# Optimization experiments

Hardware: AMD Instinct MI355X
Metric: run time of the kernel (lower is better)

## Reference

```python
import jax, jax.numpy as jnp
import numpy as np

N, E = 50000, 800000
IN_FEATS, H, F = 128, 2, 64
NEG_SLOPE = 0.2


def _gat_conv(x, W, attn_l, attn_r, bias, src, dst):
    """DGL-style GATConv. x:[N,IN], W:[H*F,IN], attn_l/attn_r:[H,F], bias:[H*F]. Returns [N,H,F]."""
    z = (x @ W.T).reshape(N, H, F)                      # node projections
    el = jnp.einsum('nhf,hf->nh', z, attn_l)            # [N,H]
    er = jnp.einsum('nhf,hf->nh', z, attn_r)            # [N,H]
    e = jax.nn.leaky_relu(el[src] + er[dst], NEG_SLOPE) # [E,H] edge logits
    # edge softmax over incoming edges of each destination node
    m = jax.ops.segment_max(e, dst, num_segments=N)     # [N,H]
    ex = jnp.exp(e - m[dst])
    s = jax.ops.segment_sum(ex, dst, num_segments=N)    # [N,H]
    alpha = ex / s[dst]                                 # [E,H]
    msg = alpha[:, :, None] * z[src]                    # [E,H,F]
    out = jax.ops.segment_sum(msg, dst, num_segments=N) # [N,H,F]
    return out + bias.reshape(1, H, F)


def setup_inputs() -> dict:
    key = jax.random.key(0)
    ks = jax.random.split(key, 10)
    x = jax.random.normal(ks[0], (N, IN_FEATS), dtype=jnp.float32)
    h = jax.random.normal(ks[1], (N, H, F), dtype=jnp.float32)
    src = jax.random.randint(ks[2], (E,), 0, N, dtype=jnp.int32)
    dst = jax.random.randint(ks[3], (E,), 0, N, dtype=jnp.int32)
    sc = 1.0 / np.sqrt(IN_FEATS)
    W = jax.random.normal(ks[4], (3, H * F, IN_FEATS), dtype=jnp.float32) * sc  # r,u,c fc weights
    attn_l = jax.random.normal(ks[5], (3, H, F), dtype=jnp.float32) * 0.1
    attn_r = jax.random.normal(ks[6], (3, H, F), dtype=jnp.float32) * 0.1
    conv_bias = jax.random.normal(ks[7], (3, H * F), dtype=jnp.float32) * 0.02
    gate_bias = jax.random.uniform(ks[8], (3, H, F), dtype=jnp.float32)  # torch.rand init
    return {"x": x, "h": h, "W": W, "attn_l": attn_l, "attn_r": attn_r,
            "conv_bias": conv_bias, "gate_bias": gate_bias, "src": src, "dst": dst}


def reference(x, h, W, attn_l, attn_r, conv_bias, gate_bias, src, dst):
    # r, u, c gates; each GATConv is applied to x (use_hidden=False branch)
    r = jax.nn.sigmoid(_gat_conv(x, W[0], attn_l[0], attn_r[0], conv_bias[0], src, dst) + gate_bias[0])
    u = jax.nn.sigmoid(_gat_conv(x, W[1], attn_l[1], attn_r[1], conv_bias[1], src, dst) + gate_bias[1])
    # note: original computes h_ = r*h but never uses it in this branch (dead code)
    c = jax.nn.sigmoid(_gat_conv(x, W[2], attn_l[2], attn_r[2], conv_bias[2], src, dst) + gate_bias[2])
    new_h = u * h + (1.0 - u) * c
    return new_h
```

## Files before the change

### kernel.cpp

```cpp
#include <hip/hip_runtime.h>
#include <hip/hip_bf16.h>
#include <math.h>

#define NN 50000
#define EE 800000
#define KIN 128
#define HFD 128
#define ZB 256
#define NB 196
#define KBG 1564
#define CAP 56
#define BSH 7

typedef __bf16 bf16_t;
typedef __bf16 bf16x8 __attribute__((ext_vector_type(8)));
typedef float f32x2 __attribute__((ext_vector_type(2)));
typedef float f32x4 __attribute__((ext_vector_type(4)));
typedef unsigned short u16;
typedef unsigned int u32;
typedef unsigned char u8;

__device__ __forceinline__ float ldf(const void* p, size_t i, int isf32) {
    return isf32 ? ((const float*)p)[i] : (float)((const bf16_t*)p)[i];
}
__device__ __forceinline__ bf16x8 load8bf(const void* base, size_t off, int isf32) {
    if (isf32) {
        const float4* p = (const float4*)((const float*)base + off);
        float4 u = p[0], v = p[1];
        bf16x8 r;
        r[0] = (bf16_t)u.x; r[1] = (bf16_t)u.y; r[2] = (bf16_t)u.z; r[3] = (bf16_t)u.w;
        r[4] = (bf16_t)v.x; r[5] = (bf16_t)v.y; r[6] = (bf16_t)v.z; r[7] = (bf16_t)v.w;
        return r;
    }
    return *(const bf16x8*)((const bf16_t*)base + off);
}

__device__ __forceinline__ uint2 pack8f(const float* v) {
    u32 lo = __builtin_amdgcn_cvt_pk_fp8_f32(v[0], v[1], 0u, false);
    lo = __builtin_amdgcn_cvt_pk_fp8_f32(v[2], v[3], lo, true);
    u32 hi = __builtin_amdgcn_cvt_pk_fp8_f32(v[4], v[5], 0u, false);
    hi = __builtin_amdgcn_cvt_pk_fp8_f32(v[6], v[7], hi, true);
    return make_uint2(lo, hi);
}

__global__ __launch_bounds__(256) void k_front(const unsigned short* __restrict__ xw,
                                               const void* __restrict__ W,
                                               const void* __restrict__ attn_l,
                                               const void* __restrict__ attn_r,
                                               u8* __restrict__ bkt,
                                               int* __restrict__ dflag,
                                               bf16_t* __restrict__ walv)
{
    const int b = blockIdx.x, tid = threadIdx.x;
    int i = b * 256 + tid;
    if (i < NN) *(int*)(bkt + ((size_t)i << BSH)) = 0;
    if (b > 8) return;

    __shared__ int cnt;
    if (tid == 0) cnt = 0;
    __syncthreads();
    int c = 0;
    for (int k = tid; k < 2048; k += 256) {
        int e = (xw[k] >> 7) & 0xFF;
        if (e > 150) c++;
    }
    atomicAdd(&cnt, c);
    __syncthreads();
    const int isf32 = (cnt > 20) ? 1 : 0;

    if (b == 0) {
        if (tid == 0) dflag[0] = isf32;
        return;
    }
    const int c8 = b - 1;
    const int side = c8 >> 2, g = (c8 >> 1) & 1, h = c8 & 1;
    const void* attn = side ? attn_r : attn_l;
    const int k = tid;
    if (k < KIN) {
        float acc = 0.f;
        for (int f = 0; f < 64; f++) {
            float wv = ldf(W, ((size_t)(g + 1) * HFD + h * 64 + f) * KIN + k, isf32);
            float av = ldf(attn, (size_t)((g + 1) * 2 + h) * 64 + f, isf32);
            acc += wv * av;
        }
        walv[(size_t)c8 * KIN + k] = (bf16_t)acc;
    }
}

__global__ __launch_bounds__(256) void k_big(const void* __restrict__ x,
                                             const void* __restrict__ W,
                                             const bf16_t* __restrict__ walv,
                                             u8* __restrict__ z8,
                                             float* __restrict__ eln,
                                             float* __restrict__ ern,
                                             const int* __restrict__ src,
                                             const int* __restrict__ dst,
                                             u8* __restrict__ bkt,
                                             const int* __restrict__ dflag)
{
    __shared__ bf16_t wlds[128 * 128];

    const int bx = blockIdx.x;
    if (bx & 1) {
        int base = (bx >> 1) * 1024 + threadIdx.x * 4;
        if (base < EE) {
            int4 s4 = *(const int4*)(src + base);
            int4 d4 = *(const int4*)(dst + base);
            u8* r0 = bkt + ((size_t)d4.x << BSH);
            u8* r1 = bkt + ((size_t)d4.y << BSH);
            u8* r2 = bkt + ((size_t)d4.z << BSH);
            u8* r3 = bkt + ((size_t)d4.w << BSH);
            int p0 = atomicAdd((int*)r0, 1);
            int p1 = atomicAdd((int*)r1, 1);
            int p2 = atomicAdd((int*)r2, 1);
            int p3 = atomicAdd((int*)r3, 1);
            if (p0 < CAP) *(u16*)(r0 + 4 + 2 * p0) = (u16)s4.x;
            if (p1 < CAP) *(u16*)(r1 + 4 + 2 * p1) = (u16)s4.y;
            if (p2 < CAP) *(u16*)(r2 + 4 + 2 * p2) = (u16)s4.z;
            if (p3 < CAP) *(u16*)(r3 + 4 + 2 * p3) = (u16)s4.w;
        }
        return;
    }

    const int isf32 = dflag[0];
    const int tid = threadIdx.x;
    const int gid = bx >> 1;
    const int g   = gid & 1;
    const int grp = gid >> 1;

    for (int c = tid; c < 2048; c += 256) {
        int col = c >> 4, g8 = c & 15;
        bf16x8 v = load8bf(W, ((size_t)(g + 1) * HFD + col) * KIN + g8 * 8, isf32);
        *(bf16x8*)(wlds + (size_t)col * 128 + (g8 ^ (col & 15)) * 8) = v;
    }

    const int wave = tid >> 6;
    const int lane = tid & 63;
    const int quad = lane >> 4;
    const int lm   = lane & 15;

    bf16x8 wb[4];
    if (g == 0) {
        if (lm < 8) {
#pragma unroll
            for (int kk = 0; kk < 4; kk++)
                wb[kk] = *(const bf16x8*)(walv + (size_t)lm * KIN + kk * 32 + quad * 8);
        } else {
#pragma unroll
            for (int kk = 0; kk < 4; kk++)
#pragma unroll
                for (int jj = 0; jj < 8; jj++) wb[kk][jj] = (bf16_t)0.f;
        }
    }

    __syncthreads();

#pragma unroll 1
    for (int m = 0; m < 2; m++) {
        const int node_base = grp * 128 + m * 64 + wave * 16;
        int nld = node_base + lm;
        if (nld > NN - 1) nld = NN - 1;

        bf16x8 a[4];
#pragma unroll
        for (int kk = 0; kk < 4; kk++)
            a[kk] = load8bf(x, (size_t)nld * KIN + kk * 32 + quad * 8, isf32);

        f32x4 acc[8];
#pragma unroll
        for (int t = 0; t < 8; t++) {
            const int wc = t * 16 + lm;
            f32x4 a4 = {0.f, 0.f, 0.f, 0.f};
#pragma unroll
            for (int kk = 0; kk < 4; kk++) {
                bf16x8 b = *(const bf16x8*)(wlds + (size_t)wc * 128 + ((kk * 4 + quad) ^ lm) * 8);
                a4 = __builtin_amdgcn_mfma_f32_16x16x32_bf16(a[kk], b, a4, 0, 0, 0);
            }
            acc[t] = a4;
        }

        if (g == 0) {
            f32x4 sacc = {0.f, 0.f, 0.f, 0.f};
#pragma unroll
            for (int kk = 0; kk < 4; kk++)
                sacc = __builtin_amdgcn_mfma_f32_16x16x32_bf16(a[kk], wb[kk], sacc, 0, 0, 0);
#pragma unroll
            for (int r = 0; r < 4; r++) {
                int nn = node_base + quad * 4 + r;
                if (nn < NN) {
                    if (lm < 4)      eln[(size_t)nn * 4 + lm] = sacc[r];
                    else if (lm < 8) ern[(size_t)nn * 4 + (lm - 4)] = sacc[r];
                }
            }
        }

#pragma unroll
        for (int r = 0; r < 4; r++) {
            float f[8];
#pragma unroll
            for (int t = 0; t < 8; t++) f[t] = acc[t][r];
            uint2 u = pack8f(f);
            int node = node_base + quad * 4 + r;
            if (node < NN)
                *(uint2*)(z8 + (size_t)node * ZB + g * 128 + lm * 8) = u;
        }
    }
}

__global__ __launch_bounds__(256) void k_agg(const u8* __restrict__ z8,
                                             const u8* __restrict__ bkt,
                                             const float* __restrict__ eln,
                                             const float* __restrict__ ern,
                                             const void* __restrict__ conv_bias,
                                             const void* __restrict__ gate_bias,
                                             const void* __restrict__ hin,
                                             void* __restrict__ out,
                                             const int* __restrict__ dflag)
{
    const int isf32 = dflag[0];
    const int wave = threadIdx.x >> 6;
    const int lane = threadIdx.x & 63;
    const int j = ((lane >> 5) << 1) | (lane & 1);
    const int n = blockIdx.x * 4 + wave;
    if (n >= NN) return;
    const u8* rb = bkt + ((size_t)n << BSH);
    int cnt = *(const int*)rb;
    if (cnt > CAP) cnt = CAP;
    const u16* row = (const u16*)(rb + 4);
    const u32* row32 = (const u32*)row;
    const float erj = ern[(size_t)n * 4 + j];
    const u32 zoff = 4 * lane;

    float a0 = 0.f, a1 = 0.f, a2 = 0.f, a3 = 0.f, s = 0.f;
    int i = 0;
    for (; i + 8 <= cnt; i += 8) {
        u32 rr[4];
#pragma unroll
        for (int q = 0; q < 4; q++) rr[q] = row32[(i >> 1) + q];
        int sn[8];
#pragma unroll
        for (int q = 0; q < 4; q++) { sn[2*q] = rr[q] & 0xFFFF; sn[2*q+1] = rr[q] >> 16; }
        u32 zb[8];
#pragma unroll
        for (int q = 0; q < 8; q++)
            zb[q] = *(const u32*)(z8 + (size_t)sn[q] * ZB + zoff);
        float w[8];
#pragma unroll
        for (int q = 0; q < 8; q++) {
            float v = eln[(size_t)sn[q] * 4 + j] + erj;
            v = v > 0.f ? v : 0.2f * v;
            w[q] = __expf(v);
        }
#pragma unroll
        for (int q = 0; q < 8; q++) {
            f32x2 lo = __builtin_amdgcn_cvt_pk_f32_fp8(zb[q], false);
            f32x2 hi = __builtin_amdgcn_cvt_pk_f32_fp8(zb[q], true);
            a0 += w[q] * lo[0];
            a1 += w[q] * lo[1];
            a2 += w[q] * hi[0];
            a3 += w[q] * hi[1];
            s += w[q];
        }
    }
    if (i + 4 <= cnt) {
        u32 rr[2];
#pragma unroll
        for (int q = 0; q < 2; q++) rr[q] = row32[(i >> 1) + q];
        int sn[4];
#pragma unroll
        for (int q = 0; q < 2; q++) { sn[2*q] = rr[q] & 0xFFFF; sn[2*q+1] = rr[q] >> 16; }
        u32 zb[4];
#pragma unroll
        for (int q = 0; q < 4; q++)
            zb[q] = *(const u32*)(z8 + (size_t)sn[q] * ZB + zoff);
#pragma unroll
        for (int q = 0; q < 4; q++) {
            float v = eln[(size_t)sn[q] * 4 + j] + erj;
            v = v > 0.f ? v : 0.2f * v;
            float w = __expf(v);
            f32x2 lo = __builtin_amdgcn_cvt_pk_f32_fp8(zb[q], false);
            f32x2 hi = __builtin_amdgcn_cvt_pk_f32_fp8(zb[q], true);
            a0 += w * lo[0];
            a1 += w * lo[1];
            a2 += w * hi[0];
            a3 += w * hi[1];
            s += w;
        }
        i += 4;
    }
    for (; i < cnt; i++) {
        int sn = row[i];
        u32 zb = *(const u32*)(z8 + (size_t)sn * ZB + zoff);
        float v = eln[(size_t)sn * 4 + j] + erj;
        v = v > 0.f ? v : 0.2f * v;
        float w = __expf(v);
        f32x2 lo = __builtin_amdgcn_cvt_pk_f32_fp8(zb, false);
        f32x2 hi = __builtin_amdgcn_cvt_pk_f32_fp8(zb, true);
        a0 += w * lo[0];
        a1 += w * lo[1];
        a2 += w * hi[0];
        a3 += w * hi[1];
        s += w;
    }

    float inv = (cnt > 0) ? 1.f / fmaxf(s, 1e-30f) : 0.f;
    float o[4] = {a0 * inv, a1 * inv, a2 * inv, a3 * inv};

    const int gate = lane >> 5;
    int cf[4];
#pragma unroll
    for (int u = 0; u < 4; u++) cf[u] = (4 * (lane & 1) + u) * 16 + ((lane & 31) >> 1);

    float res[4];
    float hh[4];
    if (lane < 32) {
#pragma unroll
        for (int u = 0; u < 4; u++)
            hh[u] = ldf(hin, (size_t)n * HFD + cf[u], isf32);
    }
#pragma unroll
    for (int u = 0; u < 4; u++) {
        float ob = ldf(conv_bias, (size_t)(gate + 1) * HFD + cf[u], isf32)
                 + ldf(gate_bias, (size_t)((gate + 1) * 2 + (lane & 1)) * 64 + (cf[u] & 63), isf32);
        float gv = 1.f / (1.f + __expf(-(o[u] + ob)));
        float other = __shfl(gv, lane ^ 32, 64);
        if (lane < 32)
            res[u] = gv * hh[u] + (1.f - gv) * other;
    }
    if (lane < 32) {
        if (isf32) {
#pragma unroll
            for (int u = 0; u < 4; u++)
                ((float*)out)[(size_t)n * HFD + cf[u]] = res[u];
        } else {
#pragma unroll
            for (int u = 0; u < 4; u++)
                ((bf16_t*)out)[(size_t)n * HFD + cf[u]] = (bf16_t)res[u];
        }
    }
}

extern "C" void kernel_launch(void* const* d_in, const int* in_sizes, int n_in,
                              void* d_out, int out_size, void* d_ws, size_t ws_size,
                              hipStream_t stream)
{
    const void* x         = d_in[0];
    const void* hin       = d_in[1];
    const void* W         = d_in[2];
    const void* attn_l    = d_in[3];
    const void* attn_r    = d_in[4];
    const void* conv_bias = d_in[5];
    const void* gate_bias = d_in[6];
    const int* src        = (const int*)d_in[7];
    const int* dst        = (const int*)d_in[8];

    char* p = (char*)d_ws;
    int* dflag    = (int*)p;    p += 256;
    u8* z8        = (u8*)p;     p += (size_t)NN * ZB;
    float* eln    = (float*)p;  p += (size_t)NN * 4 * 4;
    float* ern    = (float*)p;  p += (size_t)NN * 4 * 4;
    u8* bkt       = (u8*)p;     p += (size_t)NN << BSH;
    bf16_t* walv  = (bf16_t*)p; p += 8 * KIN * 2;

    k_front<<<NB, 256, 0, stream>>>((const unsigned short*)x, W, attn_l, attn_r,
                                    bkt, dflag, walv);
    k_big<<<KBG, 256, 0, stream>>>(x, W, walv, z8, eln, ern, src, dst,
                                   bkt, dflag);
    k_agg<<<(NN + 3) / 4, 256, 0, stream>>>(z8, bkt, eln, ern,
                                            conv_bias, gate_bias, hin, d_out, dflag);
}
```

Measured before the change: 232.6 us.

## Split GEMM blocks to 64 nodes, fold log2e into attention, use exp2 and 32-bit offsets

The projection kernel now gives each GEMM block 64 nodes instead of looping over two 64-node chunks. The grid is interleaved 2:1 GEMM-to-bucketing blocks, which doubles the GEMM block count and spreads the edge-bucketing work between them. The log2(e) factor is folded into the precomputed attention-weight vectors, so the aggregation kernel can use exp2f directly. Gather addressing also switches to 32-bit unsigned arithmetic to shave address computation. In exchange, each GEMM block pays the 32KB weight LDS fill for half as much work.

```diff
diff --git a/kernel.cpp b/kernel.cpp
--- a/kernel.cpp
+++ b/kernel.cpp
@@ -8,7 +8,8 @@
 #define HFD 128
 #define ZB 256
 #define NB 196
-#define KBG 1564
+#define GB2 1564
+#define SB 782
 #define CAP 56
 #define BSH 7
 
@@ -83,7 +84,7 @@
             float av = ldf(attn, (size_t)((g + 1) * 2 + h) * 64 + f, isf32);
             acc += wv * av;
         }
-        walv[(size_t)c8 * KIN + k] = (bf16_t)acc;
+        walv[(size_t)c8 * KIN + k] = (bf16_t)(acc * 1.44269504f);
     }
 }
 
@@ -101,8 +102,8 @@
     __shared__ bf16_t wlds[128 * 128];
 
     const int bx = blockIdx.x;
-    if (bx & 1) {
-        int base = (bx >> 1) * 1024 + threadIdx.x * 4;
+    if (bx % 3 == 2) {
+        int base = (bx / 3) * 1024 + threadIdx.x * 4;
         if (base < EE) {
             int4 s4 = *(const int4*)(src + base);
             int4 d4 = *(const int4*)(dst + base);
@@ -124,9 +125,9 @@
 
     const int isf32 = dflag[0];
     const int tid = threadIdx.x;
-    const int gid = bx >> 1;
-    const int g   = gid & 1;
-    const int grp = gid >> 1;
+    const int gid = (bx / 3) * 2 + (bx % 3);
+    const int ng = gid >> 1;
+    const int g  = gid & 1;
 
     for (int c = tid; c < 2048; c += 256) {
         int col = c >> 4, g8 = c & 15;
@@ -138,72 +139,62 @@
     const int lane = tid & 63;
     const int quad = lane >> 4;
     const int lm   = lane & 15;
-
-    bf16x8 wb[4];
+    const int node_base = ng * 64 + wave * 16;
+
+    int nld = node_base + lm;
+    if (nld > NN - 1) nld = NN - 1;
+
+    bf16x8 a[4];
+#pragma unroll
+    for (int kk = 0; kk < 4; kk++)
+        a[kk] = load8bf(x, (size_t)nld * KIN + kk * 32 + quad * 8, isf32);
+
+    __syncthreads();
+
+    f32x4 acc[8];
+#pragma unroll
+    for (int t = 0; t < 8; t++) {
+        const int wc = t * 16 + lm;
+        f32x4 a4 = {0.f, 0.f, 0.f, 0.f};
+#pragma unroll
+        for (int kk = 0; kk < 4; kk++) {
+            bf16x8 b = *(const bf16x8*)(wlds + (size_t)wc * 128 + ((kk * 4 + quad) ^ lm) * 8);
+            a4 = __builtin_amdgcn_mfma_f32_16x16x32_bf16(a[kk], b, a4, 0, 0, 0);
+        }
+        acc[t] = a4;
+    }
+
     if (g == 0) {
-        if (lm < 8) {
-#pragma unroll
-            for (int kk = 0; kk < 4; kk++)
-                wb[kk] = *(const bf16x8*)(walv + (size_t)lm * KIN + kk * 32 + quad * 8);
-        } else {
-#pragma unroll
-            for (int kk = 0; kk < 4; kk++)
-#pragma unroll
-                for (int jj = 0; jj < 8; jj++) wb[kk][jj] = (bf16_t)0.f;
-        }
-    }
-
-    __syncthreads();
-
-#pragma unroll 1
-    for (int m = 0; m < 2; m++) {
-        const int node_base = grp * 128 + m * 64 + wave * 16;
-        int nld = node_base + lm;
-        if (nld > NN - 1) nld = NN - 1;
-
-        bf16x8 a[4];
-#pragma unroll
-        for (int kk = 0; kk < 4; kk++)
-            a[kk] = load8bf(x, (size_t)nld * KIN + kk * 32 + quad * 8, isf32);
-
-        f32x4 acc[8];
-#pragma unroll
-        for (int t = 0; t < 8; t++) {
-            const int wc = t * 16 + lm;
-            f32x4 a4 = {0.f, 0.f, 0.f, 0.f};
-#pragma unroll
-            for (int kk = 0; kk < 4; kk++) {
-                bf16x8 b = *(const bf16x8*)(wlds + (size_t)wc * 128 + ((kk * 4 + quad) ^ lm) * 8);
-                a4 = __builtin_amdgcn_mfma_f32_16x16x32_bf16(a[kk], b, a4, 0, 0, 0);
+        f32x4 sacc = {0.f, 0.f, 0.f, 0.f};
+#pragma unroll
+        for (int kk = 0; kk < 4; kk++) {
+            bf16x8 b;
+            if (lm < 8) b = *(const bf16x8*)(walv + (size_t)lm * KIN + kk * 32 + quad * 8);
+            else {
+#pragma unroll
+                for (int jj = 0; jj < 8; jj++) b[jj] = (bf16_t)0.f;
             }
-            acc[t] = a4;
-        }
-
-        if (g == 0) {
-            f32x4 sacc = {0.f, 0.f, 0.f, 0.f};
-#pragma unroll
-            for (int kk = 0; kk < 4; kk++)
-                sacc = __builtin_amdgcn_mfma_f32_16x16x32_bf16(a[kk], wb[kk], sacc, 0, 0, 0);
-#pragma unroll
-            for (int r = 0; r < 4; r++) {
-                int nn = node_base + quad * 4 + r;
-                if (nn < NN) {
-                    if (lm < 4)      eln[(size_t)nn * 4 + lm] = sacc[r];
-                    else if (lm < 8) ern[(size_t)nn * 4 + (lm - 4)] = sacc[r];
-                }
+            sacc = __builtin_amdgcn_mfma_f32_16x16x32_bf16(a[kk], b, sacc, 0, 0, 0);
+        }
+#pragma unroll
+        for (int r = 0; r < 4; r++) {
+            int nn = node_base + quad * 4 + r;
+            if (nn < NN) {
+                if (lm < 4)      eln[(size_t)nn * 4 + lm] = sacc[r];
+                else if (lm < 8) ern[(size_t)nn * 4 + (lm - 4)] = sacc[r];
             }
         }
-
-#pragma unroll
-        for (int r = 0; r < 4; r++) {
-            float f[8];
-#pragma unroll
-            for (int t = 0; t < 8; t++) f[t] = acc[t][r];
-            uint2 u = pack8f(f);
-            int node = node_base + quad * 4 + r;
-            if (node < NN)
-                *(uint2*)(z8 + (size_t)node * ZB + g * 128 + lm * 8) = u;
-        }
+    }
+
+#pragma unroll
+    for (int r = 0; r < 4; r++) {
+        float f[8];
+#pragma unroll
+        for (int t = 0; t < 8; t++) f[t] = acc[t][r];
+        uint2 u = pack8f(f);
+        int node = node_base + quad * 4 + r;
+        if (node < NN)
+            *(uint2*)(z8 + (size_t)node * ZB + g * 128 + lm * 8) = u;
     }
 }
 
@@ -229,7 +220,7 @@
     const u16* row = (const u16*)(rb + 4);
     const u32* row32 = (const u32*)row;
     const float erj = ern[(size_t)n * 4 + j];
-    const u32 zoff = 4 * lane;
+    const u32 zoff = 4u * (u32)lane;
 
     float a0 = 0.f, a1 = 0.f, a2 = 0.f, a3 = 0.f, s = 0.f;
     int i = 0;
@@ -237,19 +228,19 @@
         u32 rr[4];
 #pragma unroll
         for (int q = 0; q < 4; q++) rr[q] = row32[(i >> 1) + q];
-        int sn[8];
+        u32 sn[8];
 #pragma unroll
         for (int q = 0; q < 4; q++) { sn[2*q] = rr[q] & 0xFFFF; sn[2*q+1] = rr[q] >> 16; }
         u32 zb[8];
 #pragma unroll
         for (int q = 0; q < 8; q++)
-            zb[q] = *(const u32*)(z8 + (size_t)sn[q] * ZB + zoff);
+            zb[q] = *(const u32*)(z8 + ((sn[q] << 8) + zoff));
         float w[8];
 #pragma unroll
         for (int q = 0; q < 8; q++) {
-            float v = eln[(size_t)sn[q] * 4 + j] + erj;
+            float v = eln[sn[q] * 4 + (u32)j] + erj;
             v = v > 0.f ? v : 0.2f * v;
-            w[q] = __expf(v);
+            w[q] = exp2f(v);
         }
 #pragma unroll
         for (int q = 0; q < 8; q++) {
@@ -266,18 +257,18 @@
         u32 rr[2];
 #pragma unroll
         for (int q = 0; q < 2; q++) rr[q] = row32[(i >> 1) + q];
-        int sn[4];
+        u32 sn[4];
 #pragma unroll
         for (int q = 0; q < 2; q++) { sn[2*q] = rr[q] & 0xFFFF; sn[2*q+1] = rr[q] >> 16; }
         u32 zb[4];
 #pragma unroll
         for (int q = 0; q < 4; q++)
-            zb[q] = *(const u32*)(z8 + (size_t)sn[q] * ZB + zoff);
+            zb[q] = *(const u32*)(z8 + ((sn[q] << 8) + zoff));
 #pragma unroll
         for (int q = 0; q < 4; q++) {
-            float v = eln[(size_t)sn[q] * 4 + j] + erj;
+            float v = eln[sn[q] * 4 + (u32)j] + erj;
             v = v > 0.f ? v : 0.2f * v;
-            float w = __expf(v);
+            float w = exp2f(v);
             f32x2 lo = __builtin_amdgcn_cvt_pk_f32_fp8(zb[q], false);
             f32x2 hi = __builtin_amdgcn_cvt_pk_f32_fp8(zb[q], true);
             a0 += w * lo[0];
@@ -289,11 +280,11 @@
         i += 4;
     }
     for (; i < cnt; i++) {
-        int sn = row[i];
-        u32 zb = *(const u32*)(z8 + (size_t)sn * ZB + zoff);
-        float v = eln[(size_t)sn * 4 + j] + erj;
+        u32 sn = row[i];
+        u32 zb = *(const u32*)(z8 + ((sn << 8) + zoff));
+        float v = eln[sn * 4 + (u32)j] + erj;
         v = v > 0.f ? v : 0.2f * v;
-        float w = __expf(v);
+        float w = exp2f(v);
         f32x2 lo = __builtin_amdgcn_cvt_pk_f32_fp8(zb, false);
         f32x2 hi = __builtin_amdgcn_cvt_pk_f32_fp8(zb, true);
         a0 += w * lo[0];
@@ -364,8 +355,8 @@
 
     k_front<<<NB, 256, 0, stream>>>((const unsigned short*)x, W, attn_l, attn_r,
                                     bkt, dflag, walv);
-    k_big<<<KBG, 256, 0, stream>>>(x, W, walv, z8, eln, ern, src, dst,
-                                   bkt, dflag);
+    k_big<<<GB2 + SB, 256, 0, stream>>>(x, W, walv, z8, eln, ern, src, dst,
+                                        bkt, dflag);
     k_agg<<<(NN + 3) / 4, 256, 0, stream>>>(z8, bkt, eln, ern,
                                             conv_bias, gate_bias, hin, d_out, dflag);
 }
```

After: 220.7 us. 5.1% less time.
